# Performance work log

Hardware: AMD Instinct MI355X
Metric: run time of the kernel (lower is better)

Reference implementation:

```python
import jax, jax.numpy as jnp
import numpy as np

jax.config.update("jax_enable_x64", True)  # torch casts to double for matrix_exp

EPS_DIAG = 1e-6


def setup_inputs() -> dict:
    key = jax.random.key(0)
    B, D, NB, S = 32, 128, 8, 128
    ks = jax.random.split(key, 9)
    return {
        "z0r": jax.random.normal(ks[0], (B, D), jnp.float32),
        "z0i": jax.random.normal(ks[1], (B, D), jnp.float32),
        # uniform grid: dt = time_steps[0] = 0.01, diffs == dt (uniform branch)
        "time_steps": (jnp.arange(S, dtype=jnp.float32) + 1.0) * 0.01,
        "k_coeffs": jax.random.normal(ks[2], (B, NB), jnp.float32),
        "r_coeffs": jax.random.normal(ks[3], (B, NB), jnp.float32),
        "alpha": jax.random.normal(ks[4], (B, 1), jnp.float32),
        "beta": jax.random.normal(ks[5], (B, 1), jnp.float32),
        "K_bases": jax.random.normal(ks[6], (NB, D, D), jnp.float32) * 0.01,
        "R_bases": jax.random.normal(ks[7], (NB, D, D), jnp.float32) * 0.01,
    }


def _build_generator(k_coeffs, r_coeffs, alpha, beta, K_bases, R_bases):
    # A = alpha * skew(K_sum) + beta * -(R_sum^T @ R_sum), per batch element
    K_sum = jnp.einsum("bn,nij->bij", k_coeffs, K_bases)
    R_sum = jnp.einsum("bn,nij->bij", r_coeffs, R_bases)
    skew = K_sum - jnp.swapaxes(K_sum, -1, -2)
    neg_gram = -jnp.einsum("bji,bjk->bik", R_sum, R_sum)  # -(R^T @ R)
    return alpha[..., None] * skew + beta[..., None] * neg_gram  # (B, D, D)


def _propagators(A, time_steps, uniform):
    D = A.shape[-1]
    S = time_steps.shape[0]
    if uniform:
        dt = time_steps[0]
        A64 = A.astype(jnp.float64) * dt.astype(jnp.float64) + EPS_DIAG * jnp.eye(D, dtype=jnp.float64)
        M = jax.vmap(jax.scipy.linalg.expm)(A64).astype(jnp.complex64)  # (B, D, D)
        # cumulative matrix powers M, M^2, ..., M^S via O(log S) associative scan
        Ms = jnp.broadcast_to(M[:, None], (M.shape[0], S, D, D))
        props = jax.lax.associative_scan(jnp.matmul, Ms, axis=1)
    else:
        A_t = A[:, None].astype(jnp.float64) * time_steps.astype(jnp.float64)[None, :, None, None]
        props = jax.vmap(jax.vmap(jax.scipy.linalg.expm))(A_t).astype(jnp.complex64)
    return props  # (B, S, D, D)


def reference(z0r, z0i, time_steps, k_coeffs, r_coeffs, alpha, beta, K_bases, R_bases):
    ts = np.asarray(time_steps)
    uniform = ts.shape[0] <= 1 or np.allclose(ts[1:] - ts[:-1], ts[0], atol=1e-6)
    A = _build_generator(k_coeffs, r_coeffs, alpha, beta, K_bases, R_bases)
    props = _propagators(A, time_steps, uniform)
    z = (z0r + 1j * z0i).astype(jnp.complex64)  # (B, D)
    # z_evolved[b, s, o] = sum_i z[b, i] * props[b, s, o, i]
    return jnp.einsum("bi,bsoi->bso", z, props)
```

## Files before the change

kernel.cpp:

```cpp
#include <hip/hip_runtime.h>

#define BATCH   32
#define DIM     128
#define NBASES  8
#define SSTEPS  128
#define LDA     136

typedef __attribute__((ext_vector_type(8))) short s8v;
typedef __attribute__((ext_vector_type(4))) float f4v;

__device__ __forceinline__ f4v mf(s8v a, s8v b, f4v c) {
    return __builtin_amdgcn_mfma_f32_16x16x32_bf16(a, b, c, 0, 0, 0);
}
__device__ __forceinline__ s8v ld8(const short* p) {
    return *reinterpret_cast<const s8v*>(p);
}
__device__ __forceinline__ float upbf(short h) {
    return __uint_as_float(((unsigned)(unsigned short)h) << 16);
}
__device__ __forceinline__ void splitbf(float v, short& hi, short& lo) {
    const unsigned u = __float_as_uint(v);
    hi = (short)(u >> 16);
    const float fh = __uint_as_float(u & 0xffff0000u);
    lo = (short)(__float_as_uint(v - fh) >> 16);
}

__device__ __forceinline__ void write_out(float* __restrict__ outF, int b, int sidx,
                                          int o, int c, float val,
                                          int interleaved, int out_size)
{
    if (interleaved) {
        const int oi = ((b * SSTEPS + sidx) * DIM + o) * 2 + c;
        if (oi < out_size) outF[oi] = val;
    } else if (c == 0) {
        const int oi = (b * SSTEPS + sidx) * DIM + o;
        if (oi < out_size) outF[oi] = val;
    }
}

__device__ __forceinline__ void mm_full(const short* __restrict__ Ah,
                                        const short* __restrict__ Al,
                                        const short* __restrict__ Bh,
                                        const short* __restrict__ Bl,
                                        f4v acc[2][4], int w, int lane)
{
    const int l15 = lane & 15, quad = lane >> 4;
    const int mb = (w & 3) * 32, nb = (w >> 2) * 64;
    #pragma unroll
    for (int kk = 0; kk < DIM; kk += 32) {
        const int ko = kk + quad * 8;
        const s8v a0h = ld8(Ah + (mb +      l15) * LDA + ko);
        const s8v a0l = ld8(Al + (mb +      l15) * LDA + ko);
        const s8v a1h = ld8(Ah + (mb + 16 + l15) * LDA + ko);
        const s8v a1l = ld8(Al + (mb + 16 + l15) * LDA + ko);
        #pragma unroll
        for (int ni = 0; ni < 4; ++ni) {
            const s8v bh = ld8(Bh + (nb + ni * 16 + l15) * LDA + ko);
            const s8v bl = ld8(Bl + (nb + ni * 16 + l15) * LDA + ko);
            acc[0][ni] = mf(a0h, bh, acc[0][ni]);
            acc[0][ni] = mf(a0h, bl, acc[0][ni]);
            acc[0][ni] = mf(a0l, bh, acc[0][ni]);
            acc[1][ni] = mf(a1h, bh, acc[1][ni]);
            acc[1][ni] = mf(a1h, bl, acc[1][ni]);
            acc[1][ni] = mf(a1l, bh, acc[1][ni]);
        }
    }
}

__device__ __forceinline__ void mm_rw(const short* __restrict__ Ah,
                                      const short* __restrict__ Al,
                                      const short* __restrict__ Hh,
                                      const short* __restrict__ Hl,
                                      f4v acc[2], int w, int lane)
{
    const int l15 = lane & 15, quad = lane >> 4;
    const int mb = w * 16;
    #pragma unroll
    for (int kk = 0; kk < DIM; kk += 32) {
        const int ko = kk + quad * 8;
        const s8v ah = ld8(Ah + (mb + l15) * LDA + ko);
        const s8v al = ld8(Al + (mb + l15) * LDA + ko);
        #pragma unroll
        for (int ci = 0; ci < 2; ++ci) {
            const s8v bh = ld8(Hh + (ci * 16 + l15) * LDA + ko);
            const s8v bl = ld8(Hl + (ci * 16 + l15) * LDA + ko);
            acc[ci] = mf(ah, bh, acc[ci]);
            acc[ci] = mf(ah, bl, acc[ci]);
            acc[ci] = mf(al, bh, acc[ci]);
        }
    }
}

__global__ __launch_bounds__(512, 1)
void htg_mfma(const float* __restrict__ z0r, const float* __restrict__ z0i,
              const float* __restrict__ ts,  const float* __restrict__ kco,
              const float* __restrict__ rco, const float* __restrict__ alp,
              const float* __restrict__ bet, const float* __restrict__ KB,
              const float* __restrict__ RB,  float* __restrict__ outF,
              int interleaved, int out_size)
{
    __shared__ short nm_hi[DIM * LDA], nm_lo[DIM * LDA];
    __shared__ short tr_hi[DIM * LDA], tr_lo[DIM * LDA];
    __shared__ short ht_hi[32 * LDA],  ht_lo[32 * LDA];
    __shared__ float s_z[2 * DIM];

    const int b = blockIdx.x, t = threadIdx.x;
    const int w = t >> 6, lane = t & 63;
    const int l15 = lane & 15, quad = lane >> 4;
    const f4v z4 = {0.f, 0.f, 0.f, 0.f};

    {
        float rc[NBASES], kc[NBASES];
        #pragma unroll
        for (int n = 0; n < NBASES; ++n) {
            rc[n] = rco[b * NBASES + n];
            kc[n] = kco[b * NBASES + n];
        }
        #pragma unroll
        for (int q = 0; q < 8; ++q) {
            const int e = q * 2048 + t * 4;
            float4 r4 = {0.f, 0.f, 0.f, 0.f}, k4 = {0.f, 0.f, 0.f, 0.f};
            #pragma unroll
            for (int n = 0; n < NBASES; ++n) {
                const float4 rv = *reinterpret_cast<const float4*>(RB + n * DIM * DIM + e);
                const float4 kv = *reinterpret_cast<const float4*>(KB + n * DIM * DIM + e);
                r4.x += rc[n] * rv.x; r4.y += rc[n] * rv.y;
                r4.z += rc[n] * rv.z; r4.w += rc[n] * rv.w;
                k4.x += kc[n] * kv.x; k4.y += kc[n] * kv.y;
                k4.z += kc[n] * kv.z; k4.w += kc[n] * kv.w;
            }
            const int r = e >> 7, c = e & 127;
            const float rr[4] = {r4.x, r4.y, r4.z, r4.w};
            const float kk[4] = {k4.x, k4.y, k4.z, k4.w};
            #pragma unroll
            for (int j = 0; j < 4; ++j) {
                short hi, lo;
                splitbf(rr[j], hi, lo);
                tr_hi[(c + j) * LDA + r] = hi; tr_lo[(c + j) * LDA + r] = lo;
                splitbf(kk[j], hi, lo);
                nm_hi[r * LDA + c + j] = hi;  nm_lo[r * LDA + c + j] = lo;
            }
        }
        if (t < 2 * DIM)
            s_z[t] = (t < DIM) ? z0r[b * DIM + t] : z0i[b * DIM + (t - DIM)];
    }
    __syncthreads();

    f4v acc[2][4];
    const int mb = (w & 3) * 32, nb = (w >> 2) * 64;

    #pragma unroll
    for (int i = 0; i < 2; ++i)
        #pragma unroll
        for (int j = 0; j < 4; ++j) acc[i][j] = z4;
    mm_full(tr_hi, tr_lo, tr_hi, tr_lo, acc, w, lane);
    __syncthreads();
    {
        const float alpha = alp[b], beta = bet[b], dtf = ts[0];
        #pragma unroll
        for (int mi = 0; mi < 2; ++mi)
            #pragma unroll
            for (int ni = 0; ni < 4; ++ni)
                #pragma unroll
                for (int r = 0; r < 4; ++r) {
                    const int row = mb + mi * 16 + quad * 4 + r;
                    const int col = nb + ni * 16 + l15;
                    const float k1 = upbf(nm_hi[row * LDA + col]) + upbf(nm_lo[row * LDA + col]);
                    const float k2 = upbf(nm_hi[col * LDA + row]) + upbf(nm_lo[col * LDA + row]);
                    float x = (alpha * (k1 - k2) - beta * acc[mi][ni][r]) * dtf;
                    if (row == col) x += 1e-6f;
                    acc[mi][ni][r] = x;
                }
    }
    __syncthreads();
    #pragma unroll
    for (int mi = 0; mi < 2; ++mi)
        #pragma unroll
        for (int ni = 0; ni < 4; ++ni)
            #pragma unroll
            for (int r = 0; r < 4; ++r) {
                const int row = mb + mi * 16 + quad * 4 + r;
                const int col = nb + ni * 16 + l15;
                short hi, lo;
                splitbf(acc[mi][ni][r], hi, lo);
                nm_hi[row * LDA + col] = hi; nm_lo[row * LDA + col] = lo;
                tr_hi[col * LDA + row] = hi; tr_lo[col * LDA + row] = lo;
            }
    __syncthreads();

    #pragma unroll
    for (int i = 0; i < 2; ++i)
        #pragma unroll
        for (int j = 0; j < 4; ++j) acc[i][j] = z4;
    mm_full(nm_hi, nm_lo, tr_hi, tr_lo, acc, w, lane);
    __syncthreads();
    #pragma unroll
    for (int mi = 0; mi < 2; ++mi)
        #pragma unroll
        for (int ni = 0; ni < 4; ++ni)
            #pragma unroll
            for (int r = 0; r < 4; ++r) {
                const int row = mb + mi * 16 + quad * 4 + r;
                const int col = nb + ni * 16 + l15;
                const float xv = upbf(nm_hi[row * LDA + col]) + upbf(nm_lo[row * LDA + col]);
                float v = acc[mi][ni][r] * (1.f / 24.f) + xv * (1.f / 6.f);
                if (row == col) v += 0.5f;
                short hi, lo;
                splitbf(v, hi, lo);
                tr_hi[col * LDA + row] = hi; tr_lo[col * LDA + row] = lo;
            }
    __syncthreads();

    #pragma unroll
    for (int i = 0; i < 2; ++i)
        #pragma unroll
        for (int j = 0; j < 4; ++j) acc[i][j] = z4;
    mm_full(nm_hi, nm_lo, tr_hi, tr_lo, acc, w, lane);
    __syncthreads();
    #pragma unroll
    for (int mi = 0; mi < 2; ++mi)
        #pragma unroll
        for (int ni = 0; ni < 4; ++ni)
            #pragma unroll
            for (int r = 0; r < 4; ++r) {
                const int row = mb + mi * 16 + quad * 4 + r;
                const int col = nb + ni * 16 + l15;
                float v = acc[mi][ni][r];
                if (row == col) v += 1.f;
                short hi, lo;
                splitbf(v, hi, lo);
                tr_hi[col * LDA + row] = hi; tr_lo[col * LDA + row] = lo;
            }
    __syncthreads();

    #pragma unroll
    for (int i = 0; i < 2; ++i)
        #pragma unroll
        for (int j = 0; j < 4; ++j) acc[i][j] = z4;
    mm_full(nm_hi, nm_lo, tr_hi, tr_lo, acc, w, lane);
    __syncthreads();
    #pragma unroll
    for (int mi = 0; mi < 2; ++mi)
        #pragma unroll
        for (int ni = 0; ni < 4; ++ni)
            #pragma unroll
            for (int r = 0; r < 4; ++r) {
                const int row = mb + mi * 16 + quad * 4 + r;
                const int col = nb + ni * 16 + l15;
                float v = acc[mi][ni][r];
                if (row == col) v += 1.f;
                short hi, lo;
                splitbf(v, hi, lo);
                nm_hi[row * LDA + col] = hi; nm_lo[row * LDA + col] = lo;
                tr_hi[col * LDA + row] = hi; tr_lo[col * LDA + row] = lo;
            }
    __syncthreads();

    if (t < 2 * DIM) {
        const int c = t >> 7, o = t & 127;
        float a = 0.f;
        #pragma unroll 4
        for (int i = 0; i < DIM; ++i)
            a += (upbf(tr_hi[i * LDA + o]) + upbf(tr_lo[i * LDA + o])) * s_z[c * DIM + i];
        short hi, lo;
        splitbf(a, hi, lo);
        ht_hi[(c * 16) * LDA + o] = hi;
        ht_lo[(c * 16) * LDA + o] = lo;
        write_out(outF, b, 0, o, c, a, interleaved, out_size);
    }
    __syncthreads();

    #pragma unroll
    for (int stage = 0; stage < 4; ++stage) {
        const int J = 1 << stage;
        f4v a2[2] = {z4, z4};
        mm_rw(nm_hi, nm_lo, ht_hi, ht_lo, a2, w, lane);
        __syncthreads();
        if (l15 < J) {
            #pragma unroll
            for (int ci = 0; ci < 2; ++ci)
                #pragma unroll
                for (int r = 0; r < 4; ++r) {
                    const int o = w * 16 + quad * 4 + r;
                    const float v = a2[ci][r];
                    short hi, lo;
                    splitbf(v, hi, lo);
                    ht_hi[(ci * 16 + l15 + J) * LDA + o] = hi;
                    ht_lo[(ci * 16 + l15 + J) * LDA + o] = lo;
                    write_out(outF, b, l15 + J, o, ci, v, interleaved, out_size);
                }
        }
        __syncthreads();
        #pragma unroll
        for (int i = 0; i < 2; ++i)
            #pragma unroll
            for (int j = 0; j < 4; ++j) acc[i][j] = z4;
        mm_full(nm_hi, nm_lo, tr_hi, tr_lo, acc, w, lane);
        __syncthreads();
        #pragma unroll
        for (int mi = 0; mi < 2; ++mi)
            #pragma unroll
            for (int ni = 0; ni < 4; ++ni)
                #pragma unroll
                for (int r = 0; r < 4; ++r) {
                    const int row = mb + mi * 16 + quad * 4 + r;
                    const int col = nb + ni * 16 + l15;
                    short hi, lo;
                    splitbf(acc[mi][ni][r], hi, lo);
                    nm_hi[row * LDA + col] = hi; nm_lo[row * LDA + col] = lo;
                    tr_hi[col * LDA + row] = hi; tr_lo[col * LDA + row] = lo;
                }
        __syncthreads();
    }

    for (int q = 1; q <= 7; ++q) {
        f4v a2[2] = {z4, z4};
        mm_rw(nm_hi, nm_lo, ht_hi, ht_lo, a2, w, lane);
        __syncthreads();
        #pragma unroll
        for (int ci = 0; ci < 2; ++ci)
            #pragma unroll
            for (int r = 0; r < 4; ++r) {
                const int o = w * 16 + quad * 4 + r;
                const float v = a2[ci][r];
                short hi, lo;
                splitbf(v, hi, lo);
                ht_hi[(ci * 16 + l15) * LDA + o] = hi;
                ht_lo[(ci * 16 + l15) * LDA + o] = lo;
                write_out(outF, b, 16 * q + l15, o, ci, v, interleaved, out_size);
            }
        __syncthreads();
    }
}

extern "C" void kernel_launch(void* const* d_in, const int* in_sizes, int n_in,
                              void* d_out, int out_size, void* d_ws, size_t ws_size,
                              hipStream_t stream)
{
    (void)in_sizes; (void)n_in; (void)d_ws; (void)ws_size;
    const float* z0r = (const float*)d_in[0];
    const float* z0i = (const float*)d_in[1];
    const float* ts  = (const float*)d_in[2];
    const float* kco = (const float*)d_in[3];
    const float* rco = (const float*)d_in[4];
    const float* alp = (const float*)d_in[5];
    const float* bet = (const float*)d_in[6];
    const float* KB  = (const float*)d_in[7];
    const float* RB  = (const float*)d_in[8];
    float* outF = (float*)d_out;

    const int interleaved = (out_size >= 2 * BATCH * SSTEPS * DIM) ? 1 : 0;

    htg_mfma<<<dim3(BATCH), dim3(512), 0, stream>>>(
        z0r, z0i, ts, kco, rco, alp, bet, KB, RB, outF, interleaved, out_size);
}
```

Measured before the change: 128.4 us.

## Fuse power-doubling matmuls with vector propagation and fold Taylor expm steps

Restructures the exp-and-power schedule. The matrix-vector products for each doubling stage are now issued alongside the full matrix squaring before a single barrier, which removes a sync round per stage. The Taylor evaluation of expm is shortened by seeding the accumulator with I + X + X²/2, which drops one full 128x128 matmul and its barriers. Transposed tiles are written with packed 4-short LDS stores, and the A-operand fragments are hoisted into registers for the tail loop. The initial vector is kept in the ht buffer so that outputs are shifted by one step, with the final step computed by a scalar matvec; this adds index complexity and a small numerical-order change.

```diff
diff --git a/kernel.cpp b/kernel.cpp
--- a/kernel.cpp
+++ b/kernel.cpp
@@ -7,6 +7,7 @@
 #define LDA     136
 
 typedef __attribute__((ext_vector_type(8))) short s8v;
+typedef __attribute__((ext_vector_type(4))) short s4v;
 typedef __attribute__((ext_vector_type(4))) float f4v;
 
 __device__ __forceinline__ f4v mf(s8v a, s8v b, f4v c) {
@@ -14,6 +15,9 @@
 }
 __device__ __forceinline__ s8v ld8(const short* p) {
     return *reinterpret_cast<const s8v*>(p);
+}
+__device__ __forceinline__ void st4(short* p, s4v v) {
+    *reinterpret_cast<s4v*>(p) = v;
 }
 __device__ __forceinline__ float upbf(short h) {
     return __uint_as_float(((unsigned)(unsigned short)h) << 16);
@@ -63,30 +67,6 @@
             acc[1][ni] = mf(a1h, bh, acc[1][ni]);
             acc[1][ni] = mf(a1h, bl, acc[1][ni]);
             acc[1][ni] = mf(a1l, bh, acc[1][ni]);
-        }
-    }
-}
-
-__device__ __forceinline__ void mm_rw(const short* __restrict__ Ah,
-                                      const short* __restrict__ Al,
-                                      const short* __restrict__ Hh,
-                                      const short* __restrict__ Hl,
-                                      f4v acc[2], int w, int lane)
-{
-    const int l15 = lane & 15, quad = lane >> 4;
-    const int mb = w * 16;
-    #pragma unroll
-    for (int kk = 0; kk < DIM; kk += 32) {
-        const int ko = kk + quad * 8;
-        const s8v ah = ld8(Ah + (mb + l15) * LDA + ko);
-        const s8v al = ld8(Al + (mb + l15) * LDA + ko);
-        #pragma unroll
-        for (int ci = 0; ci < 2; ++ci) {
-            const s8v bh = ld8(Hh + (ci * 16 + l15) * LDA + ko);
-            const s8v bl = ld8(Hl + (ci * 16 + l15) * LDA + ko);
-            acc[ci] = mf(ah, bh, acc[ci]);
-            acc[ci] = mf(ah, bl, acc[ci]);
-            acc[ci] = mf(al, bh, acc[ci]);
         }
     }
 }
@@ -102,12 +82,12 @@
     __shared__ short nm_hi[DIM * LDA], nm_lo[DIM * LDA];
     __shared__ short tr_hi[DIM * LDA], tr_lo[DIM * LDA];
     __shared__ short ht_hi[32 * LDA],  ht_lo[32 * LDA];
-    __shared__ float s_z[2 * DIM];
 
     const int b = blockIdx.x, t = threadIdx.x;
     const int w = t >> 6, lane = t & 63;
     const int l15 = lane & 15, quad = lane >> 4;
     const f4v z4 = {0.f, 0.f, 0.f, 0.f};
+    const int mb = (w & 3) * 32, nb = (w >> 2) * 64;
 
     {
         float rc[NBASES], kc[NBASES];
@@ -132,22 +112,28 @@
             const int r = e >> 7, c = e & 127;
             const float rr[4] = {r4.x, r4.y, r4.z, r4.w};
             const float kk[4] = {k4.x, k4.y, k4.z, k4.w};
+            s4v kh, kl;
             #pragma unroll
             for (int j = 0; j < 4; ++j) {
                 short hi, lo;
                 splitbf(rr[j], hi, lo);
                 tr_hi[(c + j) * LDA + r] = hi; tr_lo[(c + j) * LDA + r] = lo;
                 splitbf(kk[j], hi, lo);
-                nm_hi[r * LDA + c + j] = hi;  nm_lo[r * LDA + c + j] = lo;
-            }
-        }
-        if (t < 2 * DIM)
-            s_z[t] = (t < DIM) ? z0r[b * DIM + t] : z0i[b * DIM + (t - DIM)];
+                kh[j] = hi; kl[j] = lo;
+            }
+            st4(&nm_hi[r * LDA + c], kh);
+            st4(&nm_lo[r * LDA + c], kl);
+        }
+        if (t < 2 * DIM) {
+            const int c = t >> 7, o = t & 127;
+            const float zv = (c == 0) ? z0r[b * DIM + o] : z0i[b * DIM + o];
+            short hi, lo; splitbf(zv, hi, lo);
+            ht_hi[c * LDA + o] = hi; ht_lo[c * LDA + o] = lo;
+        }
     }
     __syncthreads();
 
     f4v acc[2][4];
-    const int mb = (w & 3) * 32, nb = (w >> 2) * 64;
 
     #pragma unroll
     for (int i = 0; i < 2; ++i)
@@ -176,18 +162,24 @@
     #pragma unroll
     for (int mi = 0; mi < 2; ++mi)
         #pragma unroll
-        for (int ni = 0; ni < 4; ++ni)
-            #pragma unroll
-            for (int r = 0; r < 4; ++r) {
-                const int row = mb + mi * 16 + quad * 4 + r;
-                const int col = nb + ni * 16 + l15;
+        for (int ni = 0; ni < 4; ++ni) {
+            const int row0 = mb + mi * 16 + quad * 4;
+            const int col  = nb + ni * 16 + l15;
+            s4v h4, l4;
+            #pragma unroll
+            for (int r = 0; r < 4; ++r) {
                 short hi, lo;
                 splitbf(acc[mi][ni][r], hi, lo);
-                nm_hi[row * LDA + col] = hi; nm_lo[row * LDA + col] = lo;
-                tr_hi[col * LDA + row] = hi; tr_lo[col * LDA + row] = lo;
-            }
-    __syncthreads();
-
+                nm_hi[(row0 + r) * LDA + col] = hi;
+                nm_lo[(row0 + r) * LDA + col] = lo;
+                h4[r] = hi; l4[r] = lo;
+            }
+            st4(&tr_hi[col * LDA + row0], h4);
+            st4(&tr_lo[col * LDA + row0], l4);
+        }
+    __syncthreads();
+
+    float a1v[2][4][4];
     #pragma unroll
     for (int i = 0; i < 2; ++i)
         #pragma unroll
@@ -197,139 +189,164 @@
     #pragma unroll
     for (int mi = 0; mi < 2; ++mi)
         #pragma unroll
+        for (int ni = 0; ni < 4; ++ni) {
+            const int row0 = mb + mi * 16 + quad * 4;
+            const int col  = nb + ni * 16 + l15;
+            s4v h4, l4;
+            #pragma unroll
+            for (int r = 0; r < 4; ++r) {
+                const int row = row0 + r;
+                const float xv = upbf(nm_hi[row * LDA + col]) + upbf(nm_lo[row * LDA + col]);
+                const float cv = acc[mi][ni][r];
+                a1v[mi][ni][r] = ((row == col) ? 1.f : 0.f) + xv + 0.5f * cv;
+                const float a2 = xv * (1.f / 6.f) + cv * (1.f / 24.f);
+                short hi, lo;
+                splitbf(cv, hi, lo);
+                nm_hi[row * LDA + col] = hi;
+                nm_lo[row * LDA + col] = lo;
+                splitbf(a2, hi, lo);
+                h4[r] = hi; l4[r] = lo;
+            }
+            st4(&tr_hi[col * LDA + row0], h4);
+            st4(&tr_lo[col * LDA + row0], l4);
+        }
+    __syncthreads();
+
+    #pragma unroll
+    for (int mi = 0; mi < 2; ++mi)
+        #pragma unroll
         for (int ni = 0; ni < 4; ++ni)
             #pragma unroll
-            for (int r = 0; r < 4; ++r) {
-                const int row = mb + mi * 16 + quad * 4 + r;
-                const int col = nb + ni * 16 + l15;
-                const float xv = upbf(nm_hi[row * LDA + col]) + upbf(nm_lo[row * LDA + col]);
-                float v = acc[mi][ni][r] * (1.f / 24.f) + xv * (1.f / 6.f);
-                if (row == col) v += 0.5f;
-                short hi, lo;
-                splitbf(v, hi, lo);
-                tr_hi[col * LDA + row] = hi; tr_lo[col * LDA + row] = lo;
-            }
-    __syncthreads();
-
-    #pragma unroll
-    for (int i = 0; i < 2; ++i)
-        #pragma unroll
-        for (int j = 0; j < 4; ++j) acc[i][j] = z4;
+            for (int r = 0; r < 4; ++r) acc[mi][ni][r] = a1v[mi][ni][r];
     mm_full(nm_hi, nm_lo, tr_hi, tr_lo, acc, w, lane);
     __syncthreads();
     #pragma unroll
     for (int mi = 0; mi < 2; ++mi)
         #pragma unroll
-        for (int ni = 0; ni < 4; ++ni)
-            #pragma unroll
-            for (int r = 0; r < 4; ++r) {
-                const int row = mb + mi * 16 + quad * 4 + r;
-                const int col = nb + ni * 16 + l15;
-                float v = acc[mi][ni][r];
-                if (row == col) v += 1.f;
-                short hi, lo;
-                splitbf(v, hi, lo);
-                tr_hi[col * LDA + row] = hi; tr_lo[col * LDA + row] = lo;
-            }
-    __syncthreads();
-
-    #pragma unroll
-    for (int i = 0; i < 2; ++i)
-        #pragma unroll
-        for (int j = 0; j < 4; ++j) acc[i][j] = z4;
-    mm_full(nm_hi, nm_lo, tr_hi, tr_lo, acc, w, lane);
-    __syncthreads();
-    #pragma unroll
-    for (int mi = 0; mi < 2; ++mi)
-        #pragma unroll
-        for (int ni = 0; ni < 4; ++ni)
-            #pragma unroll
-            for (int r = 0; r < 4; ++r) {
-                const int row = mb + mi * 16 + quad * 4 + r;
-                const int col = nb + ni * 16 + l15;
-                float v = acc[mi][ni][r];
-                if (row == col) v += 1.f;
-                short hi, lo;
-                splitbf(v, hi, lo);
-                nm_hi[row * LDA + col] = hi; nm_lo[row * LDA + col] = lo;
-                tr_hi[col * LDA + row] = hi; tr_lo[col * LDA + row] = lo;
-            }
-    __syncthreads();
+        for (int ni = 0; ni < 4; ++ni) {
+            const int row0 = mb + mi * 16 + quad * 4;
+            const int col  = nb + ni * 16 + l15;
+            s4v h4, l4;
+            #pragma unroll
+            for (int r = 0; r < 4; ++r) {
+                short hi, lo;
+                splitbf(acc[mi][ni][r], hi, lo);
+                nm_hi[(row0 + r) * LDA + col] = hi;
+                nm_lo[(row0 + r) * LDA + col] = lo;
+                h4[r] = hi; l4[r] = lo;
+            }
+            st4(&tr_hi[col * LDA + row0], h4);
+            st4(&tr_lo[col * LDA + row0], l4);
+        }
+    __syncthreads();
+
+    #pragma unroll
+    for (int stage = 0; stage < 4; ++stage) {
+        const int J = 1 << stage;
+        f4v ar = z4;
+        #pragma unroll
+        for (int i = 0; i < 2; ++i)
+            #pragma unroll
+            for (int j = 0; j < 4; ++j) acc[i][j] = z4;
+        #pragma unroll
+        for (int kk = 0; kk < DIM; kk += 32) {
+            const int ko = kk + quad * 8;
+            const s8v rah = ld8(nm_hi + (w * 16 + l15) * LDA + ko);
+            const s8v ral = ld8(nm_lo + (w * 16 + l15) * LDA + ko);
+            const s8v rbh = ld8(ht_hi + l15 * LDA + ko);
+            const s8v rbl = ld8(ht_lo + l15 * LDA + ko);
+            ar = mf(rah, rbh, ar);
+            ar = mf(rah, rbl, ar);
+            ar = mf(ral, rbh, ar);
+        }
+        mm_full(nm_hi, nm_lo, tr_hi, tr_lo, acc, w, lane);
+        __syncthreads();
+        if (l15 < 2 * J) {
+            const int o0 = w * 16 + quad * 4;
+            const int sidx = (l15 >> 1) + J - 1;
+            s4v h4, l4;
+            #pragma unroll
+            for (int r = 0; r < 4; ++r) {
+                short hi, lo;
+                splitbf(ar[r], hi, lo);
+                h4[r] = hi; l4[r] = lo;
+                write_out(outF, b, sidx, o0 + r, l15 & 1, ar[r], interleaved, out_size);
+            }
+            st4(&ht_hi[(l15 + 2 * J) * LDA + o0], h4);
+            st4(&ht_lo[(l15 + 2 * J) * LDA + o0], l4);
+        }
+        #pragma unroll
+        for (int mi = 0; mi < 2; ++mi)
+            #pragma unroll
+            for (int ni = 0; ni < 4; ++ni) {
+                const int row0 = mb + mi * 16 + quad * 4;
+                const int col  = nb + ni * 16 + l15;
+                s4v h4, l4;
+                #pragma unroll
+                for (int r = 0; r < 4; ++r) {
+                    short hi, lo;
+                    splitbf(acc[mi][ni][r], hi, lo);
+                    nm_hi[(row0 + r) * LDA + col] = hi;
+                    nm_lo[(row0 + r) * LDA + col] = lo;
+                    h4[r] = hi; l4[r] = lo;
+                }
+                st4(&tr_hi[col * LDA + row0], h4);
+                st4(&tr_lo[col * LDA + row0], l4);
+            }
+        __syncthreads();
+    }
+
+    s8v vah[4], val[4];
+    #pragma unroll
+    for (int k4 = 0; k4 < 4; ++k4) {
+        const int ko = k4 * 32 + quad * 8;
+        vah[k4] = ld8(nm_hi + (w * 16 + l15) * LDA + ko);
+        val[k4] = ld8(nm_lo + (w * 16 + l15) * LDA + ko);
+    }
+    for (int q = 1; q <= 7; ++q) {
+        f4v a2[2] = {z4, z4};
+        #pragma unroll
+        for (int k4 = 0; k4 < 4; ++k4) {
+            const int ko = k4 * 32 + quad * 8;
+            #pragma unroll
+            for (int ci = 0; ci < 2; ++ci) {
+                const s8v bh = ld8(ht_hi + (ci * 16 + l15) * LDA + ko);
+                const s8v bl = ld8(ht_lo + (ci * 16 + l15) * LDA + ko);
+                a2[ci] = mf(vah[k4], bh, a2[ci]);
+                a2[ci] = mf(vah[k4], bl, a2[ci]);
+                a2[ci] = mf(val[k4], bh, a2[ci]);
+            }
+        }
+        __syncthreads();
+        const int o0 = w * 16 + quad * 4;
+        #pragma unroll
+        for (int ci = 0; ci < 2; ++ci) {
+            const int n = ci * 16 + l15;
+            const int sidx = 16 * q + (n >> 1) - 1;
+            s4v h4, l4;
+            #pragma unroll
+            for (int r = 0; r < 4; ++r) {
+                short hi, lo;
+                splitbf(a2[ci][r], hi, lo);
+                h4[r] = hi; l4[r] = lo;
+                write_out(outF, b, sidx, o0 + r, n & 1, a2[ci][r], interleaved, out_size);
+            }
+            if (q < 7 || n < 2) {
+                st4(&ht_hi[n * LDA + o0], h4);
+                st4(&ht_lo[n * LDA + o0], l4);
+            }
+        }
+        __syncthreads();
+    }
 
     if (t < 2 * DIM) {
         const int c = t >> 7, o = t & 127;
         float a = 0.f;
         #pragma unroll 4
         for (int i = 0; i < DIM; ++i)
-            a += (upbf(tr_hi[i * LDA + o]) + upbf(tr_lo[i * LDA + o])) * s_z[c * DIM + i];
-        short hi, lo;
-        splitbf(a, hi, lo);
-        ht_hi[(c * 16) * LDA + o] = hi;
-        ht_lo[(c * 16) * LDA + o] = lo;
-        write_out(outF, b, 0, o, c, a, interleaved, out_size);
-    }
-    __syncthreads();
-
-    #pragma unroll
-    for (int stage = 0; stage < 4; ++stage) {
-        const int J = 1 << stage;
-        f4v a2[2] = {z4, z4};
-        mm_rw(nm_hi, nm_lo, ht_hi, ht_lo, a2, w, lane);
-        __syncthreads();
-        if (l15 < J) {
-            #pragma unroll
-            for (int ci = 0; ci < 2; ++ci)
-                #pragma unroll
-                for (int r = 0; r < 4; ++r) {
-                    const int o = w * 16 + quad * 4 + r;
-                    const float v = a2[ci][r];
-                    short hi, lo;
-                    splitbf(v, hi, lo);
-                    ht_hi[(ci * 16 + l15 + J) * LDA + o] = hi;
-                    ht_lo[(ci * 16 + l15 + J) * LDA + o] = lo;
-                    write_out(outF, b, l15 + J, o, ci, v, interleaved, out_size);
-                }
-        }
-        __syncthreads();
-        #pragma unroll
-        for (int i = 0; i < 2; ++i)
-            #pragma unroll
-            for (int j = 0; j < 4; ++j) acc[i][j] = z4;
-        mm_full(nm_hi, nm_lo, tr_hi, tr_lo, acc, w, lane);
-        __syncthreads();
-        #pragma unroll
-        for (int mi = 0; mi < 2; ++mi)
-            #pragma unroll
-            for (int ni = 0; ni < 4; ++ni)
-                #pragma unroll
-                for (int r = 0; r < 4; ++r) {
-                    const int row = mb + mi * 16 + quad * 4 + r;
-                    const int col = nb + ni * 16 + l15;
-                    short hi, lo;
-                    splitbf(acc[mi][ni][r], hi, lo);
-                    nm_hi[row * LDA + col] = hi; nm_lo[row * LDA + col] = lo;
-                    tr_hi[col * LDA + row] = hi; tr_lo[col * LDA + row] = lo;
-                }
-        __syncthreads();
-    }
-
-    for (int q = 1; q <= 7; ++q) {
-        f4v a2[2] = {z4, z4};
-        mm_rw(nm_hi, nm_lo, ht_hi, ht_lo, a2, w, lane);
-        __syncthreads();
-        #pragma unroll
-        for (int ci = 0; ci < 2; ++ci)
-            #pragma unroll
-            for (int r = 0; r < 4; ++r) {
-                const int o = w * 16 + quad * 4 + r;
-                const float v = a2[ci][r];
-                short hi, lo;
-                splitbf(v, hi, lo);
-                ht_hi[(ci * 16 + l15) * LDA + o] = hi;
-                ht_lo[(ci * 16 + l15) * LDA + o] = lo;
-                write_out(outF, b, 16 * q + l15, o, ci, v, interleaved, out_size);
-            }
-        __syncthreads();
+            a += (upbf(tr_hi[i * LDA + o]) + upbf(tr_lo[i * LDA + o]))
+               * (upbf(ht_hi[c * LDA + i]) + upbf(ht_lo[c * LDA + i]));
+        write_out(outF, b, 127, o, c, a, interleaved, out_size);
     }
 }
 
```

New measurement: 122.4 us. 1.05x faster.
